# Kernel optimization log

Hardware: AMD Instinct MI355X
Metric: run time of the kernel (lower is better)

The kernel has to match this reference:

```python
import jax, jax.numpy as jnp
from jax import lax
import numpy as np

HEADS = 4
BUCKET = 64
DEPTH = 4


def _conv(x, w, b):
    y = lax.conv_general_dilated(x, w, (1, 1), [(1, 1), (1, 1)],
                                 dimension_numbers=('NCHW', 'OIHW', 'NCHW'))
    return y + b[None, :, None, None]


def _convT(x, w, b):
    # torch ConvTranspose2d(k=4, s=2, p=1): flip kernel, swap io, lhs_dilation=2, pad k-1-p=2
    wk = jnp.flip(w, (2, 3)).transpose(1, 0, 2, 3)
    y = lax.conv_general_dilated(x, wk, (1, 1), [(2, 2), (2, 2)], lhs_dilation=(2, 2),
                                 dimension_numbers=('NCHW', 'OIHW', 'NCHW'))
    return y + b[None, :, None, None]


def _maxpool(x):
    return lax.reduce_window(x, -jnp.inf, lax.max, (1, 1, 2, 2), (1, 1, 2, 2), 'VALID')


def _ln(x, g, b):
    m = x.mean(-1, keepdims=True)
    v = ((x - m) ** 2).mean(-1, keepdims=True)
    return (x - m) / jnp.sqrt(v + 1e-5) * g + b


def _lsh_attention(x, Wqk, bqk, Wv, bv, Wo, bo, rot):
    # shared-QK LSH bucketed attention (single hash round), look-one-back chunks
    B, N, D = x.shape
    h, dh = HEADS, D // HEADS
    qk = (x @ Wqk + bqk).reshape(B, N, h, dh).transpose(0, 2, 1, 3)  # B h N dh
    v = (x @ Wv + bv).reshape(B, N, h, dh).transpose(0, 2, 1, 3)
    k = qk / (jnp.linalg.norm(qk, axis=-1, keepdims=True) + 1e-6)    # keys = normalized queries
    rotated = jnp.einsum('bhnd,hdr->bhnr', qk, rot)
    buckets = jnp.argmax(jnp.concatenate([rotated, -rotated], -1), -1)  # B h N
    ticker = jnp.arange(N)
    perm = jnp.argsort(buckets * N + ticker, axis=-1)  # stable sort by bucket
    inv_perm = jnp.argsort(perm, axis=-1)
    g = lambda t: jnp.take_along_axis(t, perm[..., None], axis=2)
    nc = N // BUCKET
    bq = g(qk).reshape(B, h, nc, BUCKET, dh)
    bk = g(k).reshape(B, h, nc, BUCKET, dh)
    bv_ = g(v).reshape(B, h, nc, BUCKET, dh)
    bk2 = jnp.concatenate([bk, jnp.roll(bk, 1, axis=2)], axis=3)   # look one chunk back
    bv2 = jnp.concatenate([bv_, jnp.roll(bv_, 1, axis=2)], axis=3)
    dots = jnp.einsum('bhcid,bhcjd->bhcij', bq, bk2) * (dh ** -0.5)
    spos = jnp.take_along_axis(jnp.broadcast_to(ticker, buckets.shape), perm, -1).reshape(B, h, nc, BUCKET)
    kpos = jnp.concatenate([spos, jnp.roll(spos, 1, axis=2)], axis=3)
    dots = jnp.where(spos[..., :, None] == kpos[..., None, :], -1e5, dots)  # mask self (q == k)
    attn = jax.nn.softmax(dots, -1)
    o = jnp.einsum('bhcij,bhcjd->bhcid', attn, bv2).reshape(B, h, N, dh)
    o = jnp.take_along_axis(o, inv_perm[..., None], axis=2)  # unsort
    return o.transpose(0, 2, 1, 3).reshape(B, N, D) @ Wo + bo


def _reformer(seq, ln1_g, ln1_b, Wqk, bqk, Wv, bv, Wo, bo, rot, ln2_g, ln2_b, Wff1, bff1, Wff2, bff2):
    for i in range(DEPTH):
        seq = seq + _lsh_attention(_ln(seq, ln1_g[i], ln1_b[i]), Wqk[i], bqk[i], Wv[i], bv[i], Wo[i], bo[i], rot[i])
        hdn = jax.nn.gelu(_ln(seq, ln2_g[i], ln2_b[i]) @ Wff1[i] + bff1[i])
        seq = seq + hdn @ Wff2[i] + bff2[i]
    return seq


def _forward(burst, conv1_w, conv1_b, conv2_w, conv2_b, conv3_w, conv3_b,
             ln1_g, ln1_b, Wqk, bqk, Wv, bv, Wo, bo, rot, ln2_g, ln2_b,
             Wff1, bff1, Wff2, bff2, up1_w, up1_b, dec1_w, dec1_b,
             up2_w, up2_b, dec2_w, dec2_b, out_w, out_b):
    B, T, C, H, W = burst.shape
    x = burst.reshape(B * T, C, H, W)
    e1 = jax.nn.relu(_conv(x, conv1_w, conv1_b))
    p1 = _maxpool(e1)
    e2 = jax.nn.relu(_conv(p1, conv2_w, conv2_b))
    p2 = _maxpool(e2)
    bm = jax.nn.relu(_conv(p2, conv3_w, conv3_b))
    D = bm.shape[1]
    Hq, Wq = H // 4, W // 4
    seq = bm.transpose(0, 2, 3, 1).reshape(B * T, Hq * Wq, D)
    seq = _reformer(seq, ln1_g, ln1_b, Wqk, bqk, Wv, bv, Wo, bo, rot, ln2_g, ln2_b, Wff1, bff1, Wff2, bff2)
    bm = seq.reshape(B * T, Hq, Wq, D).transpose(0, 3, 1, 2)
    d1 = _convT(bm, up1_w, up1_b)
    d1 = jax.nn.relu(_conv(jnp.concatenate([d1, e2], 1), dec1_w, dec1_b))
    d2 = _convT(d1, up2_w, up2_b)
    d2 = jax.nn.relu(_conv(jnp.concatenate([d2, e1], 1), dec2_w, dec2_b))
    sharp = jax.nn.sigmoid(_conv(d2, out_w, out_b))
    return sharp.reshape(B, T, C, H, W)[:, 0]


def setup_inputs() -> dict:
    key = jax.random.key(0)
    ks = jax.random.split(key, 20)
    s = 0.05
    n = lambda k, shape: jax.random.normal(k, shape, jnp.float32) * s
    inp = {}
    inp['burst'] = jax.random.uniform(ks[0], (1, 7, 3, 256, 256), jnp.float32)
    inp['conv1_w'] = n(ks[1], (64, 3, 3, 3)); inp['conv1_b'] = jnp.zeros((64,), jnp.float32)
    inp['conv2_w'] = n(ks[2], (128, 64, 3, 3)); inp['conv2_b'] = jnp.zeros((128,), jnp.float32)
    inp['conv3_w'] = n(ks[3], (256, 128, 3, 3)); inp['conv3_b'] = jnp.zeros((256,), jnp.float32)
    inp['ln1_g'] = jnp.ones((4, 256), jnp.float32); inp['ln1_b'] = jnp.zeros((4, 256), jnp.float32)
    inp['Wqk'] = n(ks[4], (4, 256, 256)); inp['bqk'] = jnp.zeros((4, 256), jnp.float32)
    inp['Wv'] = n(ks[5], (4, 256, 256)); inp['bv'] = jnp.zeros((4, 256), jnp.float32)
    inp['Wo'] = n(ks[6], (4, 256, 256)); inp['bo'] = jnp.zeros((4, 256), jnp.float32)
    inp['rot'] = jax.random.normal(ks[7], (4, 4, 64, 32), jnp.float32)  # depth, heads, d_head, n_buckets//2
    inp['ln2_g'] = jnp.ones((4, 256), jnp.float32); inp['ln2_b'] = jnp.zeros((4, 256), jnp.float32)
    inp['Wff1'] = n(ks[8], (4, 256, 1024)); inp['bff1'] = jnp.zeros((4, 1024), jnp.float32)
    inp['Wff2'] = n(ks[9], (4, 1024, 256)); inp['bff2'] = jnp.zeros((4, 256), jnp.float32)
    inp['up1_w'] = n(ks[10], (256, 128, 4, 4)); inp['up1_b'] = jnp.zeros((128,), jnp.float32)
    inp['dec1_w'] = n(ks[11], (128, 256, 3, 3)); inp['dec1_b'] = jnp.zeros((128,), jnp.float32)
    inp['up2_w'] = n(ks[12], (128, 64, 4, 4)); inp['up2_b'] = jnp.zeros((64,), jnp.float32)
    inp['dec2_w'] = n(ks[13], (64, 128, 3, 3)); inp['dec2_b'] = jnp.zeros((64,), jnp.float32)
    inp['out_w'] = n(ks[14], (3, 64, 3, 3)); inp['out_b'] = jnp.zeros((3,), jnp.float32)
    return inp


def reference(burst, conv1_w, conv1_b, conv2_w, conv2_b, conv3_w, conv3_b,
              ln1_g, ln1_b, Wqk, bqk, Wv, bv, Wo, bo, rot, ln2_g, ln2_b,
              Wff1, bff1, Wff2, bff2, up1_w, up1_b, dec1_w, dec1_b,
              up2_w, up2_b, dec2_w, dec2_b, out_w, out_b):
    return _forward(burst, conv1_w, conv1_b, conv2_w, conv2_b, conv3_w, conv3_b,
                    ln1_g, ln1_b, Wqk, bqk, Wv, bv, Wo, bo, rot, ln2_g, ln2_b,
                    Wff1, bff1, Wff2, bff2, up1_w, up1_b, dec1_w, dec1_b,
                    up2_w, up2_b, dec2_w, dec2_b, out_w, out_b)
```

## Files before the change

### kernel.cpp

```cpp
#include <hip/hip_runtime.h>
#include <hip/hip_bf16.h>
#include <math.h>

using short8  = __attribute__((ext_vector_type(8))) short;
using half8   = __attribute__((ext_vector_type(8))) _Float16;
using floatx4 = __attribute__((ext_vector_type(4))) float;

static __device__ __forceinline__ float gelu_f(float x) {
    float x3 = x * x * x;
    return 0.5f * x * (1.f + tanhf(0.7978845608028654f * (x + 0.044715f * x3)));
}
static __device__ __forceinline__ short f2h(float f) {
    _Float16 h = (_Float16)f;
    return __builtin_bit_cast(short, h);
}
static __device__ __forceinline__ short f2bf(float f) {
    unsigned u = __float_as_uint(f);
    u += 0x7fffu + ((u >> 16) & 1u);
    return (short)(u >> 16);
}
static __device__ __forceinline__ float bf2f(short s) {
    return __uint_as_float(((unsigned)(unsigned short)s) << 16);
}
struct bf3s { short a, b, c; };
static __device__ __forceinline__ bf3s split3(float v) {
    short c0 = f2bf(v); float r = v - bf2f(c0);
    short c1 = f2bf(r); r -= bf2f(c1);
    short c2 = f2bf(r);
    bf3s s; s.a = c0; s.b = c1; s.c = c2; return s;
}

template <int OCB>
__global__ __launch_bounds__(256) void conv1_nhwc_kernel(
    const float* __restrict__ in1, const float* __restrict__ w,
    const float* __restrict__ bias, float* __restrict__ out, int H, int W, int OC)
{
    int tx = threadIdx.x, ty = threadIdx.y;
    int x = blockIdx.x * 16 + tx, y = blockIdx.y * 16 + ty;
    int oc0 = blockIdx.z * OCB;
    const int C = 3;
    float acc[OCB];
#pragma unroll
    for (int o = 0; o < OCB; ++o) acc[o] = 0.f;
    for (int ic = 0; ic < C; ++ic) {
        const float* src = in1 + (size_t)ic * H * W;
        float v[9];
#pragma unroll
        for (int ky = 0; ky < 3; ++ky) {
            int iy = y + ky - 1;
            bool okY = (iy >= 0) && (iy < H);
#pragma unroll
            for (int kx = 0; kx < 3; ++kx) {
                int ix = x + kx - 1;
                bool ok = okY && (ix >= 0) && (ix < W);
                v[ky * 3 + kx] = ok ? src[(size_t)iy * W + ix] : 0.f;
            }
        }
        const float* wp = w + ((size_t)oc0 * C + ic) * 9;
#pragma unroll
        for (int o = 0; o < OCB; ++o) {
            const float* wo = wp + (size_t)o * C * 9;
            acc[o] += v[0]*wo[0] + v[1]*wo[1] + v[2]*wo[2]
                    + v[3]*wo[3] + v[4]*wo[4] + v[5]*wo[5]
                    + v[6]*wo[6] + v[7]*wo[7] + v[8]*wo[8];
        }
    }
    float* op = out + ((size_t)y * W + x) * OC + oc0;
#pragma unroll
    for (int o = 0; o < OCB; ++o)
        op[o] = fmaxf(acc[o] + bias[oc0 + o], 0.f);
}

__global__ __launch_bounds__(256) void maxpool1_bf3_kernel(
    const float* __restrict__ in, short* __restrict__ o0, short* __restrict__ o1,
    short* __restrict__ o2, int OW, int IW, int C)
{
    int idx = blockIdx.x * 256 + threadIdx.x;
    int g = idx % (C >> 2); int p = idx / (C >> 2);
    int x = p % OW; int y = p / OW;
    size_t base = ((size_t)(2 * y) * IW + 2 * x) * C + g * 4;
    float4 a = *(const float4*)(in + base);
    float4 b = *(const float4*)(in + base + C);
    float4 c = *(const float4*)(in + base + (size_t)IW * C);
    float4 d = *(const float4*)(in + base + (size_t)IW * C + C);
    float v[4];
    v[0] = fmaxf(fmaxf(a.x, b.x), fmaxf(c.x, d.x));
    v[1] = fmaxf(fmaxf(a.y, b.y), fmaxf(c.y, d.y));
    v[2] = fmaxf(fmaxf(a.z, b.z), fmaxf(c.z, d.z));
    v[3] = fmaxf(fmaxf(a.w, b.w), fmaxf(c.w, d.w));
    size_t o = (size_t)p * C + g * 4;
#pragma unroll
    for (int j = 0; j < 4; ++j) {
        bf3s s = split3(v[j]);
        o0[o + j] = s.a; o1[o + j] = s.b; o2[o + j] = s.c;
    }
}

__global__ __launch_bounds__(256) void maxpool2_bf3_kernel(
    const short* __restrict__ i0, const short* __restrict__ i1,
    const short* __restrict__ i2, short* __restrict__ o0, short* __restrict__ o1,
    short* __restrict__ o2, int OW, int IW, int C)
{
    int idx = blockIdx.x * 256 + threadIdx.x;
    int g = idx % (C >> 2); int p = idx / (C >> 2);
    int x = p % OW; int y = p / OW;
    float v[4] = {-1e30f, -1e30f, -1e30f, -1e30f};
#pragma unroll
    for (int dy = 0; dy < 2; ++dy)
#pragma unroll
        for (int dx = 0; dx < 2; ++dx) {
            size_t base = ((size_t)(2 * y + dy) * IW + 2 * x + dx) * C + g * 4;
#pragma unroll
            for (int j = 0; j < 4; ++j) {
                float u = bf2f(i0[base + j]) + bf2f(i1[base + j]) + bf2f(i2[base + j]);
                v[j] = fmaxf(v[j], u);
            }
        }
    size_t o = (size_t)p * C + g * 4;
#pragma unroll
    for (int j = 0; j < 4; ++j) {
        bf3s s = split3(v[j]);
        o0[o + j] = s.a; o1[o + j] = s.b; o2[o + j] = s.c;
    }
}

__global__ void pack_conv3_kernel(const float* __restrict__ w,
                                  short* __restrict__ B0, short* __restrict__ B1,
                                  short* __restrict__ B2, int C, int OC, int total)
{
    int t = blockIdx.x * 256 + threadIdx.x;
    if (t >= total) return;
    int lane = t & 63, fi = t >> 6;
    int NT = OC >> 4;
    int nt = fi % NT, kt = fi / NT;
    int cpt = C >> 5;
    int tap = kt / cpt, ct = kt % cpt;
    int c = ct * 32 + (lane >> 4) * 8;
    int oc = nt * 16 + (lane & 15);
    short8 v0, v1, v2;
#pragma unroll
    for (int j = 0; j < 8; ++j) {
        bf3s s = split3(w[((size_t)oc * C + c + j) * 9 + tap]);
        v0[j] = s.a; v1[j] = s.b; v2[j] = s.c;
    }
    ((short8*)B0)[t] = v0; ((short8*)B1)[t] = v1; ((short8*)B2)[t] = v2;
}

__global__ __launch_bounds__(256) void conv_bf3_kernel(
    const short* __restrict__ ia0, const short* __restrict__ ia1,
    const short* __restrict__ ia2,
    const short* __restrict__ B0, const short* __restrict__ B1,
    const short* __restrict__ B2, const float* __restrict__ bias,
    float* __restrict__ outf, short* __restrict__ o0, short* __restrict__ o1,
    short* __restrict__ o2, short* __restrict__ oh,
    int H, int W, int C, int OC)
{
    int tid = threadIdx.x, wave = tid >> 6, lane = tid & 63;
    int quad = lane >> 4, l16 = lane & 15;
    int x0 = blockIdx.x * 64, y = blockIdx.y, nt0 = blockIdx.z * 4;
    int cpt = C >> 5, NT = OC >> 4;
    const short8* b0p = (const short8*)B0;
    const short8* b1p = (const short8*)B1;
    const short8* b2p = (const short8*)B2;
    floatx4 aM[4] = {{0,0,0,0},{0,0,0,0},{0,0,0,0},{0,0,0,0}};
    floatx4 aC[4] = {{0,0,0,0},{0,0,0,0},{0,0,0,0},{0,0,0,0}};
    int xm = x0 + wave * 16 + l16;
    for (int ky = 0; ky < 3; ++ky) {
        int yy = y + ky - 1;
        bool rok = (yy >= 0) && (yy < H);
        for (int kx = 0; kx < 3; ++kx) {
            int xx = xm + kx - 1;
            bool ok = rok && (xx >= 0) && (xx < W);
            size_t pos = (size_t)yy * W + xx;
            int ktb = (ky * 3 + kx) * cpt;
            for (int ct = 0; ct < cpt; ++ct) {
                int cc = ct * 32 + quad * 8;
                short8 A0 = {0,0,0,0,0,0,0,0}, A1 = A0, A2 = A0;
                if (ok) {
                    A0 = *(const short8*)(ia0 + pos * C + cc);
                    A1 = *(const short8*)(ia1 + pos * C + cc);
                    A2 = *(const short8*)(ia2 + pos * C + cc);
                }
                size_t bi = ((size_t)(ktb + ct) * NT + nt0) * 64 + lane;
#pragma unroll
                for (int s = 0; s < 4; ++s) {
                    short8 w0 = b0p[bi + s * 64];
                    short8 w1 = b1p[bi + s * 64];
                    short8 w2 = b2p[bi + s * 64];
                    aM[s] = __builtin_amdgcn_mfma_f32_16x16x32_bf16(A0, w0, aM[s], 0, 0, 0);
                    aC[s] = __builtin_amdgcn_mfma_f32_16x16x32_bf16(A0, w1, aC[s], 0, 0, 0);
                    aC[s] = __builtin_amdgcn_mfma_f32_16x16x32_bf16(A1, w0, aC[s], 0, 0, 0);
                    aC[s] = __builtin_amdgcn_mfma_f32_16x16x32_bf16(A0, w2, aC[s], 0, 0, 0);
                    aC[s] = __builtin_amdgcn_mfma_f32_16x16x32_bf16(A1, w1, aC[s], 0, 0, 0);
                    aC[s] = __builtin_amdgcn_mfma_f32_16x16x32_bf16(A2, w0, aC[s], 0, 0, 0);
                }
            }
        }
    }
#pragma unroll
    for (int s = 0; s < 4; ++s) {
        int n = (nt0 + s) * 16 + l16;
        float bs = bias[n];
#pragma unroll
        for (int r = 0; r < 4; ++r) {
            int m = wave * 16 + quad * 4 + r;
            int x = x0 + m;
            float v = fmaxf(aM[s][r] + aC[s][r] + bs, 0.f);
            size_t o = ((size_t)y * W + x) * OC + n;
            if (outf) outf[o] = v;
            else {
                bf3s sp = split3(v);
                o0[o] = sp.a; o1[o] = sp.b; o2[o] = sp.c;
                oh[o] = f2h(v);
            }
        }
    }
}

__global__ __launch_bounds__(256) void ln_bf3_kernel(
    const float* __restrict__ x, const float* __restrict__ g,
    const float* __restrict__ b, short* __restrict__ y0,
    short* __restrict__ y1, short* __restrict__ y2)
{
    int wave = threadIdx.x >> 6, lane = threadIdx.x & 63;
    int n = blockIdx.x * 4 + wave;
    const float* xr = x + (size_t)n * 256;
    float4 v = *(const float4*)(xr + lane * 4);
    float s = v.x + v.y + v.z + v.w;
#pragma unroll
    for (int m = 1; m < 64; m <<= 1) s += __shfl_xor(s, m);
    float mean = s * (1.f / 256.f);
    float cx = v.x - mean, cy = v.y - mean, cz = v.z - mean, cw = v.w - mean;
    float q = cx * cx + cy * cy + cz * cz + cw * cw;
#pragma unroll
    for (int m = 1; m < 64; m <<= 1) q += __shfl_xor(q, m);
    float rstd = rsqrtf(q * (1.f / 256.f) + 1e-5f);
    float4 gv = *(const float4*)(g + lane * 4);
    float4 bv = *(const float4*)(b + lane * 4);
    float o[4];
    o[0] = cx * rstd * gv.x + bv.x;
    o[1] = cy * rstd * gv.y + bv.y;
    o[2] = cz * rstd * gv.z + bv.z;
    o[3] = cw * rstd * gv.w + bv.w;
    size_t ob = (size_t)n * 256 + lane * 4;
#pragma unroll
    for (int j = 0; j < 4; ++j) {
        bf3s sp = split3(o[j]);
        y0[ob + j] = sp.a; y1[ob + j] = sp.b; y2[ob + j] = sp.c;
    }
}

__global__ __launch_bounds__(256) void bucketn_kernel(
    const float* __restrict__ qk, const float* __restrict__ rot,
    int* __restrict__ buckets, float* __restrict__ knrm)
{
    int t = blockIdx.x * 256 + threadIdx.x;
    int h = t >> 12, n = t & 4095;
    const float* q = qk + (size_t)n * 256 + h * 64;
    const float* R = rot + (size_t)h * 2048;
    float acc[32];
#pragma unroll
    for (int r = 0; r < 32; ++r) acc[r] = 0.f;
    float s2 = 0.f;
    for (int d = 0; d < 64; ++d) {
        float qd = q[d];
        s2 += qd * qd;
        const float* Rd = R + d * 32;
#pragma unroll
        for (int r = 0; r < 32; ++r) acc[r] += qd * Rd[r];
    }
    knrm[t] = 1.f / (sqrtf(s2) + 1e-6f);
    float bvv = acc[0]; int best = 0;
#pragma unroll
    for (int j = 1; j < 64; ++j) {
        float val = (j < 32) ? acc[j] : -acc[j - 32];
        if (val > bvv) { bvv = val; best = j; }
    }
    buckets[t] = best;
}

__global__ __launch_bounds__(256) void lsh_sort_kernel(
    const int* __restrict__ buckets, int* __restrict__ perm)
{
    int h = blockIdx.x;
    const int* bk = buckets + h * 4096;
    __shared__ unsigned long long mask[64][64];
    __shared__ int counts[64];
    __shared__ int offsets[64];
    __shared__ int wpre[64][64];
    int tid = threadIdx.x, wave = tid >> 6, lane = tid & 63;
    for (int w = wave * 16; w < wave * 16 + 16; ++w) {
        int bl = bk[w * 64 + lane];
        for (int b = 0; b < 64; ++b) {
            unsigned long long m = __ballot(bl == b);
            if (lane == b) mask[b][w] = m;
        }
    }
    __syncthreads();
    if (tid < 64) {
        int c = 0;
        for (int w = 0; w < 64; ++w) c += __popcll(mask[tid][w]);
        counts[tid] = c;
    }
    __syncthreads();
    if (tid == 0) {
        int a = 0;
        for (int b = 0; b < 64; ++b) { offsets[b] = a; a += counts[b]; }
    }
    __syncthreads();
    for (int b = wave * 16; b < wave * 16 + 16; ++b) {
        int c = __popcll(mask[b][lane]);
        int incl = c;
#pragma unroll
        for (int off = 1; off < 64; off <<= 1) {
            int nb = __shfl_up(incl, off);
            if (lane >= off) incl += nb;
        }
        wpre[b][lane] = incl - c + offsets[b];
    }
    __syncthreads();
    for (int i = tid; i < 4096; i += 256) {
        int b = bk[i]; int w = i >> 6; int l = i & 63;
        unsigned long long below = mask[b][w] & ((1ull << l) - 1ull);
        int pos = wpre[b][w] + __popcll(below);
        perm[h * 4096 + pos] = i;
    }
}

__global__ __launch_bounds__(256) void attn_kernel(
    const float* __restrict__ qk, const float* __restrict__ vv,
    const float* __restrict__ knrm, const int* __restrict__ perm,
    short* __restrict__ o0, short* __restrict__ o1, short* __restrict__ o2)
{
    __shared__ float ks[128 * 64];
    __shared__ float dotsT[128 * 64];
    int c = blockIdx.x, h = blockIdx.y;
    int tid = threadIdx.x;
    const int* pm = perm + h * 4096;
    int cm = (c + 63) & 63;
    {
        int jr = tid >> 1, hf = tid & 1;
        int sk = (jr < 64) ? (c * 64 + jr) : (cm * 64 + (jr - 64));
        int nk = pm[sk];
        float sc = knrm[h * 4096 + nk];
        const float* src = qk + (size_t)nk * 256 + h * 64 + hf * 32;
        float* dst = ks + jr * 64 + hf * 32;
#pragma unroll
        for (int d = 0; d < 32; d += 4) {
            float4 v = *(const float4*)(src + d);
            v.x *= sc; v.y *= sc; v.z *= sc; v.w *= sc;
            *(float4*)(dst + d) = v;
        }
    }
    __syncthreads();
    int r = tid & 63, jg = tid >> 6;
    int nq = pm[c * 64 + r];
    {
        float qreg[64];
        const float* src = qk + (size_t)nq * 256 + h * 64;
#pragma unroll
        for (int d = 0; d < 64; d += 4) {
            float4 v = *(const float4*)(src + d);
            qreg[d] = v.x; qreg[d + 1] = v.y; qreg[d + 2] = v.z; qreg[d + 3] = v.w;
        }
        for (int j = jg * 32; j < jg * 32 + 32; ++j) {
            const float* kr = ks + j * 64;
            float dot = 0.f;
#pragma unroll
            for (int d = 0; d < 64; ++d) dot += qreg[d] * kr[d];
            int sk = (j < 64) ? (c * 64 + j) : (cm * 64 + (j - 64));
            int nk = pm[sk];
            dot = (nk == nq) ? -1e5f : dot * 0.125f;
            dotsT[j * 64 + r] = dot;
        }
    }
    __syncthreads();
    {
        int jr = tid >> 1, hf = tid & 1;
        int sk = (jr < 64) ? (c * 64 + jr) : (cm * 64 + (jr - 64));
        int nk = pm[sk];
        const float* src = vv + (size_t)nk * 256 + h * 64 + hf * 32;
        float* dst = ks + jr * 64 + hf * 32;
#pragma unroll
        for (int d = 0; d < 32; d += 4)
            *(float4*)(dst + d) = *(const float4*)(src + d);
    }
    if (tid < 64) {
        int rr = tid;
        float mx = -1e30f;
        for (int j = 0; j < 128; ++j) mx = fmaxf(mx, dotsT[j * 64 + rr]);
        float s = 0.f;
        for (int j = 0; j < 128; ++j) {
            float e = expf(dotsT[j * 64 + rr] - mx);
            dotsT[j * 64 + rr] = e; s += e;
        }
        float inv = 1.f / s;
        for (int j = 0; j < 128; ++j) dotsT[j * 64 + rr] *= inv;
    }
    __syncthreads();
    int dg = jg;
    float acc[16];
#pragma unroll
    for (int d = 0; d < 16; ++d) acc[d] = 0.f;
    for (int j = 0; j < 128; ++j) {
        float a = dotsT[j * 64 + r];
        const float* vr = ks + j * 64 + dg * 16;
#pragma unroll
        for (int d = 0; d < 16; ++d) acc[d] += a * vr[d];
    }
    size_t ob = (size_t)nq * 256 + h * 64 + dg * 16;
#pragma unroll
    for (int d = 0; d < 16; ++d) {
        bf3s sp = split3(acc[d]);
        o0[ob + d] = sp.a; o1[ob + d] = sp.b; o2[ob + d] = sp.c;
    }
}

static __device__ __forceinline__ void pack_one(
    const float* __restrict__ W, short* __restrict__ B0, short* __restrict__ B1,
    short* __restrict__ B2, int N, int t)
{
    int lane = t & 63, fi = t >> 6;
    int NT = N >> 4;
    int nt = fi % NT, kt = fi / NT;
    int n = nt * 16 + (lane & 15);
    int k0 = kt * 32 + (lane >> 4) * 8;
    short8 v0, v1, v2;
#pragma unroll
    for (int j = 0; j < 8; ++j) {
        bf3s s = split3(W[(size_t)(k0 + j) * N + n]);
        v0[j] = s.a; v1[j] = s.b; v2[j] = s.c;
    }
    ((short8*)B0)[t] = v0; ((short8*)B1)[t] = v1; ((short8*)B2)[t] = v2;
}

__global__ void pack_layer_kernel(
    const float* __restrict__ Wqk, const float* __restrict__ Wv,
    const float* __restrict__ Wo, const float* __restrict__ Wff1,
    const float* __restrict__ Wff2,
    short* q0, short* q1, short* q2, short* v0, short* v1, short* v2,
    short* o0, short* o1, short* o2, short* f10, short* f11, short* f12,
    short* f20, short* f21, short* f22)
{
    int t = blockIdx.x * 256 + threadIdx.x;
    if (t < 8192)       pack_one(Wqk, q0, q1, q2, 256, t);
    else if (t < 16384) pack_one(Wv, v0, v1, v2, 256, t - 8192);
    else if (t < 24576) pack_one(Wo, o0, o1, o2, 256, t - 16384);
    else if (t < 57344) pack_one(Wff1, f10, f11, f12, 1024, t - 24576);
    else if (t < 90112) pack_one(Wff2, f20, f21, f22, 256, t - 57344);
}

static __device__ __forceinline__ void gemm_bf3_core(
    const short* __restrict__ A0, const short* __restrict__ A1,
    const short* __restrict__ A2,
    const short* __restrict__ B0, const short* __restrict__ B1,
    const short* __restrict__ B2, const float* __restrict__ bias,
    float* __restrict__ Cf, short* __restrict__ D0, short* __restrict__ D1,
    short* __restrict__ D2, int N, int K, int act, int resid, int bx, int by)
{
    int tid = threadIdx.x, wave = tid >> 6, lane = tid & 63;
    int quad = lane >> 4, l16 = lane & 15;
    int m0 = by * 64 + wave * 16;
    int NT = N >> 4, nt0 = bx * 2;
    size_t arow = (size_t)(m0 + l16) * K + quad * 8;
    const short8* b0p = (const short8*)B0;
    const short8* b1p = (const short8*)B1;
    const short8* b2p = (const short8*)B2;
    floatx4 aM0 = {0,0,0,0}, aM1 = {0,0,0,0};
    floatx4 aC10 = {0,0,0,0}, aC11 = {0,0,0,0};
    floatx4 aC20 = {0,0,0,0}, aC21 = {0,0,0,0};
    int KT = K >> 5;
    size_t bi0 = (size_t)nt0 * 64 + lane;
    short8 a0 = *(const short8*)(A0 + arow);
    short8 a1 = *(const short8*)(A1 + arow);
    short8 a2 = *(const short8*)(A2 + arow);
    short8 w00 = b0p[bi0], w01 = b1p[bi0], w02 = b2p[bi0];
    short8 w10 = b0p[bi0 + 64], w11 = b1p[bi0 + 64], w12 = b2p[bi0 + 64];
    for (int kt = 0; kt < KT; ++kt) {
        short8 na0 = {}, na1 = {}, na2 = {};
        short8 nw00 = {}, nw01 = {}, nw02 = {}, nw10 = {}, nw11 = {}, nw12 = {};
        if (kt + 1 < KT) {
            size_t ar = arow + (size_t)(kt + 1) * 32;
            na0 = *(const short8*)(A0 + ar);
            na1 = *(const short8*)(A1 + ar);
            na2 = *(const short8*)(A2 + ar);
            size_t nbi = ((size_t)(kt + 1) * NT + nt0) * 64 + lane;
            nw00 = b0p[nbi]; nw01 = b1p[nbi]; nw02 = b2p[nbi];
            nw10 = b0p[nbi + 64]; nw11 = b1p[nbi + 64]; nw12 = b2p[nbi + 64];
        }
        aM0  = __builtin_amdgcn_mfma_f32_16x16x32_bf16(a0, w00, aM0, 0, 0, 0);
        aM1  = __builtin_amdgcn_mfma_f32_16x16x32_bf16(a0, w10, aM1, 0, 0, 0);
        aC10 = __builtin_amdgcn_mfma_f32_16x16x32_bf16(a0, w01, aC10, 0, 0, 0);
        aC11 = __builtin_amdgcn_mfma_f32_16x16x32_bf16(a0, w11, aC11, 0, 0, 0);
        aC20 = __builtin_amdgcn_mfma_f32_16x16x32_bf16(a1, w00, aC20, 0, 0, 0);
        aC21 = __builtin_amdgcn_mfma_f32_16x16x32_bf16(a1, w10, aC21, 0, 0, 0);
        aC10 = __builtin_amdgcn_mfma_f32_16x16x32_bf16(a0, w02, aC10, 0, 0, 0);
        aC11 = __builtin_amdgcn_mfma_f32_16x16x32_bf16(a0, w12, aC11, 0, 0, 0);
        aC20 = __builtin_amdgcn_mfma_f32_16x16x32_bf16(a1, w01, aC20, 0, 0, 0);
        aC21 = __builtin_amdgcn_mfma_f32_16x16x32_bf16(a1, w11, aC21, 0, 0, 0);
        aC10 = __builtin_amdgcn_mfma_f32_16x16x32_bf16(a2, w00, aC10, 0, 0, 0);
        aC11 = __builtin_amdgcn_mfma_f32_16x16x32_bf16(a2, w10, aC11, 0, 0, 0);
        a0 = na0; a1 = na1; a2 = na2;
        w00 = nw00; w01 = nw01; w02 = nw02;
        w10 = nw10; w11 = nw11; w12 = nw12;
    }
    floatx4 aM[2] = {aM0, aM1};
    floatx4 c1[2] = {aC10, aC11};
    floatx4 c2[2] = {aC20, aC21};
#pragma unroll
    for (int s = 0; s < 2; ++s) {
        int n = (nt0 + s) * 16 + l16;
        float bs = bias[n];
#pragma unroll
        for (int r = 0; r < 4; ++r) {
            int m = m0 + quad * 4 + r;
            float v = aM[s][r] + (c1[s][r] + c2[s][r]) + bs;
            if (act == 1) v = gelu_f(v);
            size_t o = (size_t)m * N + n;
            if (D0) {
                bf3s sp = split3(v);
                D0[o] = sp.a; D1[o] = sp.b; D2[o] = sp.c;
            } else {
                if (resid) v += Cf[o];
                Cf[o] = v;
            }
        }
    }
}

__global__ __launch_bounds__(256) void gemm_bf3_kernel(
    const short* A0, const short* A1, const short* A2,
    const short* B0, const short* B1, const short* B2,
    const float* bias, float* Cf, short* D0, short* D1, short* D2,
    int N, int K, int act, int resid)
{
    gemm_bf3_core(A0, A1, A2, B0, B1, B2, bias, Cf, D0, D1, D2,
                  N, K, act, resid, blockIdx.x, blockIdx.y);
}

__global__ __launch_bounds__(256) void gemm_qkv_bf3_kernel(
    const short* A0, const short* A1, const short* A2,
    const short* Q0, const short* Q1, const short* Q2,
    const float* qb, float* Cq,
    const short* V0, const short* V1, const short* V2,
    const float* vb, float* Cv, int K)
{
    int side = blockIdx.x >> 3;
    gemm_bf3_core(A0, A1, A2, side ? V0 : Q0, side ? V1 : Q1, side ? V2 : Q2,
                  side ? vb : qb, side ? Cv : Cq, nullptr, nullptr, nullptr,
                  256, K, 0, 0, blockIdx.x & 7, blockIdx.y);
}

__global__ void pack_conv_kernel(const float* __restrict__ w, short* __restrict__ Bp,
                                 int C, int OC, int NT, int total)
{
    int t = blockIdx.x * 256 + threadIdx.x;
    if (t >= total) return;
    int lane = t & 63, fi = t >> 6;
    int nt = fi % NT, kt = fi / NT;
    int cpt = C >> 5;
    int tap = kt / cpt, ct = kt % cpt;
    int c = ct * 32 + (lane >> 4) * 8;
    int oc = nt * 16 + (lane & 15);
    short8 v;
#pragma unroll
    for (int j = 0; j < 8; ++j) {
        float f = (oc < OC) ? w[((size_t)oc * C + c + j) * 9 + tap] : 0.f;
        v[j] = f2h(f);
    }
    ((short8*)Bp)[t] = v;
}

__global__ void pack_convt_kernel(const float* __restrict__ w, short* __restrict__ Bp,
                                  int IC, int OC, int total)
{
    int t = blockIdx.x * 256 + threadIdx.x;
    if (t >= total) return;
    int lane = t & 63, fi = t >> 6;
    int NT = OC >> 4, cpt = IC >> 5, KT4 = 4 * cpt;
    int nt = fi % NT, r = fi / NT;
    int kt = r % KT4, pz = r / KT4;
    int py = pz >> 1, px = pz & 1;
    int t4 = kt / cpt, ct = kt % cpt;
    int ty = t4 >> 1, tx = t4 & 1;
    int ky = py ? (2 * ty) : (1 + 2 * ty);
    int kx = px ? (2 * tx) : (1 + 2 * tx);
    int ic = ct * 32 + (lane >> 4) * 8;
    int oc = nt * 16 + (lane & 15);
    short8 v;
#pragma unroll
    for (int j = 0; j < 8; ++j)
        v[j] = f2h(w[(((size_t)(ic + j) * OC + oc) * 4 + ky) * 4 + kx]);
    ((short8*)Bp)[t] = v;
}

__global__ __launch_bounds__(256) void conv_mfma_kernel(
    const short* __restrict__ in1, int C1, const short* __restrict__ in2, int C2,
    const short* __restrict__ Bp, const float* __restrict__ bias,
    short* __restrict__ outb, int H, int W, int OC)
{
    int tid = threadIdx.x, wave = tid >> 6, lane = tid & 63;
    int quad = lane >> 4, l16 = lane & 15;
    int x0 = blockIdx.x * 64, y = blockIdx.y, nt0 = blockIdx.z * 4;
    int C = C1 + C2, cpt = C >> 5, NT = OC >> 4;
    const half8* bp = (const half8*)Bp;
    floatx4 acc[4] = {{0,0,0,0},{0,0,0,0},{0,0,0,0},{0,0,0,0}};
    int xm = x0 + wave * 16 + l16;
    for (int ky = 0; ky < 3; ++ky) {
        int yy = y + ky - 1;
        bool rok = (yy >= 0) && (yy < H);
        for (int kx = 0; kx < 3; ++kx) {
            int xx = xm + kx - 1;
            bool ok = rok && (xx >= 0) && (xx < W);
            size_t pos = (size_t)yy * W + xx;
            int ktb = (ky * 3 + kx) * cpt;
            for (int ct = 0; ct < cpt; ++ct) {
                int cc = ct * 32 + quad * 8;
                half8 a = {};
                if (ok) {
                    const short* src = (cc < C1) ? (in1 + pos * C1 + cc)
                                                 : (in2 + pos * C2 + (cc - C1));
                    a = *(const half8*)src;
                }
                size_t bi = ((size_t)(ktb + ct) * NT + nt0) * 64 + lane;
#pragma unroll
                for (int s = 0; s < 4; ++s)
                    acc[s] = __builtin_amdgcn_mfma_f32_16x16x32_f16(a, bp[bi + s * 64], acc[s], 0, 0, 0);
            }
        }
    }
#pragma unroll
    for (int s = 0; s < 4; ++s) {
        int n = (nt0 + s) * 16 + l16;
        float bs = bias[n];
#pragma unroll
        for (int r = 0; r < 4; ++r) {
            int m = wave * 16 + quad * 4 + r;
            int x = x0 + m;
            float v = fmaxf(acc[s][r] + bs, 0.f);
            outb[((size_t)y * W + x) * OC + n] = f2h(v);
        }
    }
}

__global__ __launch_bounds__(256) void convt_mfma_kernel(
    const short* __restrict__ in, int IC, const short* __restrict__ Bp,
    const float* __restrict__ bias, short* __restrict__ outb, int IH, int IW, int OC)
{
    int tid = threadIdx.x, wave = tid >> 6, lane = tid & 63;
    int quad = lane >> 4, l16 = lane & 15;
    int pz = blockIdx.z & 3, nt0 = (blockIdx.z >> 2) * 4;
    int py = pz >> 1, px = pz & 1;
    int a0 = blockIdx.y, b0 = blockIdx.x * 64;
    int cpt = IC >> 5, NT = OC >> 4, KT4 = 4 * cpt;
    const half8* bp = (const half8*)Bp;
    floatx4 acc[4] = {{0,0,0,0},{0,0,0,0},{0,0,0,0},{0,0,0,0}};
    int bm = b0 + wave * 16 + l16;
    for (int ty = 0; ty < 2; ++ty) {
        int iy = a0 + (py ? (1 - ty) : (-ty));
        bool rok = (iy >= 0) && (iy < IH);
        for (int tx = 0; tx < 2; ++tx) {
            int ix = bm + (px ? (1 - tx) : (-tx));
            bool ok = rok && (ix >= 0) && (ix < IW);
            size_t pos = (size_t)iy * IW + ix;
            int ktb = (ty * 2 + tx) * cpt;
            for (int ct = 0; ct < cpt; ++ct) {
                int cc = ct * 32 + quad * 8;
                half8 a = {};
                if (ok) a = *(const half8*)(in + pos * IC + cc);
                size_t bi = ((size_t)(pz * KT4 + ktb + ct) * NT + nt0) * 64 + lane;
#pragma unroll
                for (int s = 0; s < 4; ++s)
                    acc[s] = __builtin_amdgcn_mfma_f32_16x16x32_f16(a, bp[bi + s * 64], acc[s], 0, 0, 0);
            }
        }
    }
    int OW = IW * 2;
    int oy = 2 * a0 + py;
#pragma unroll
    for (int s = 0; s < 4; ++s) {
        int n = (nt0 + s) * 16 + l16;
        float bs = bias[n];
#pragma unroll
        for (int r = 0; r < 4; ++r) {
            int m = wave * 16 + quad * 4 + r;
            int ox = 2 * (b0 + m) + px;
            outb[((size_t)oy * OW + ox) * OC + n] = f2h(acc[s][r] + bs);
        }
    }
}

__global__ __launch_bounds__(256) void convout_mfma_kernel(
    const short* __restrict__ in, const short* __restrict__ Bp,
    const float* __restrict__ bias, float* __restrict__ out, int H, int W)
{
    int tid = threadIdx.x, wave = tid >> 6, lane = tid & 63;
    int quad = lane >> 4, l16 = lane & 15;
    int x0 = blockIdx.x * 64, y = blockIdx.y;
    const int C = 64, cpt = 2;
    const half8* bp = (const half8*)Bp;
    floatx4 acc = {0,0,0,0};
    int xm = x0 + wave * 16 + l16;
    for (int ky = 0; ky < 3; ++ky) {
        int yy = y + ky - 1;
        bool rok = (yy >= 0) && (yy < H);
        for (int kx = 0; kx < 3; ++kx) {
            int xx = xm + kx - 1;
            bool ok = rok && (xx >= 0) && (xx < W);
            size_t pos = (size_t)yy * W + xx;
            int ktb = (ky * 3 + kx) * cpt;
#pragma unroll
            for (int ct = 0; ct < cpt; ++ct) {
                int cc = ct * 32 + quad * 8;
                half8 a = {};
                if (ok) a = *(const half8*)(in + pos * C + cc);
                acc = __builtin_amdgcn_mfma_f32_16x16x32_f16(
                          a, bp[(size_t)(ktb + ct) * 64 + lane], acc, 0, 0, 0);
            }
        }
    }
    int oc = l16;
    if (oc < 3) {
        float bs = bias[oc];
#pragma unroll
        for (int r = 0; r < 4; ++r) {
            int m = wave * 16 + quad * 4 + r;
            int x = x0 + m;
            float v = acc[r] + bs;
            out[(size_t)oc * H * W + (size_t)y * W + x] = 1.f / (1.f + expf(-v));
        }
    }
}

__global__ __launch_bounds__(256) void f2h_kernel(
    const float* __restrict__ in, short* __restrict__ out, int n)
{
    int i = blockIdx.x * 256 + threadIdx.x;
    if (i < n) out[i] = f2h(in[i]);
}

extern "C" void kernel_launch(void* const* d_in, const int* in_sizes, int n_in,
                              void* d_out, int out_size, void* d_ws, size_t ws_size,
                              hipStream_t stream)
{
    const float* burst   = (const float*)d_in[0];
    const float* conv1_w = (const float*)d_in[1];  const float* conv1_b = (const float*)d_in[2];
    const float* conv2_w = (const float*)d_in[3];  const float* conv2_b = (const float*)d_in[4];
    const float* conv3_w = (const float*)d_in[5];  const float* conv3_b = (const float*)d_in[6];
    const float* ln1_g   = (const float*)d_in[7];  const float* ln1_b   = (const float*)d_in[8];
    const float* Wqk     = (const float*)d_in[9];  const float* bqk     = (const float*)d_in[10];
    const float* Wv      = (const float*)d_in[11]; const float* bvv     = (const float*)d_in[12];
    const float* Wo      = (const float*)d_in[13]; const float* bo      = (const float*)d_in[14];
    const float* rot     = (const float*)d_in[15];
    const float* ln2_g   = (const float*)d_in[16]; const float* ln2_b   = (const float*)d_in[17];
    const float* Wff1    = (const float*)d_in[18]; const float* bff1    = (const float*)d_in[19];
    const float* Wff2    = (const float*)d_in[20]; const float* bff2    = (const float*)d_in[21];
    const float* up1_w   = (const float*)d_in[22]; const float* up1_b   = (const float*)d_in[23];
    const float* dec1_w  = (const float*)d_in[24]; const float* dec1_b  = (const float*)d_in[25];
    const float* up2_w   = (const float*)d_in[26]; const float* up2_b   = (const float*)d_in[27];
    const float* dec2_w  = (const float*)d_in[28]; const float* dec2_b  = (const float*)d_in[29];
    const float* out_w   = (const float*)d_in[30]; const float* out_b   = (const float*)d_in[31];

    float* ws = (float*)d_ws;
    short* e1h = (short*)(ws + 0);
    short* e2h = (short*)(ws + 2097152);
    float* seq = ws + 3145728;
    float* qkb = ws + 4194304;
    float* vvb = ws + 5242880;
    float* knb = ws + 6291456;
    int* buckets = (int*)(ws + 6307840);
    int* perm    = (int*)(ws + 6324224);
    short* xn0 = (short*)(ws + 6340608);
    short* xn1 = (short*)(ws + 6864896);
    short* xn2 = (short*)(ws + 7389184);
    short* hdn0 = (short*)(ws + 7913472);
    short* hdn1 = (short*)(ws + 10010624);
    short* hdn2 = (short*)(ws + 12107776);
    short* pqk0 = (short*)(ws + 14204928); short* pqk1 = (short*)(ws + 14237696); short* pqk2 = (short*)(ws + 14270464);
    short* pv0  = (short*)(ws + 14303232); short* pv1  = (short*)(ws + 14336000); short* pv2  = (short*)(ws + 14368768);
    short* po0  = (short*)(ws + 14401536); short* po1  = (short*)(ws + 14434304); short* po2  = (short*)(ws + 14467072);
    short* pf10 = (short*)(ws + 14499840); short* pf11 = (short*)(ws + 14630912); short* pf12 = (short*)(ws + 14761984);
    short* pf20 = (short*)(ws + 14893056); short* pf21 = (short*)(ws + 15024128); short* pf22 = (short*)(ws + 15155200);
    short* pdec1 = (short*)(ws + 15286272);
    short* pdec2 = (short*)(ws + 15433728);
    short* pout  = (short*)(ws + 15470592);
    short* pup1  = (short*)(ws + 15475200);
    short* pup2  = (short*)(ws + 15737344);
    float* e1f = ws + 7913472;
    short* p1_0 = (short*)(ws + 12107776); short* p1_1 = (short*)(ws + 12632064); short* p1_2 = (short*)(ws + 13156352);
    short* p2_0 = (short*)(ws + 13680640); short* p2_1 = (short*)(ws + 13942784); short* p2_2 = (short*)(ws + 14204928);
    short* pc2_0 = (short*)(ws + 14467072); short* pc2_1 = (short*)(ws + 14503936); short* pc2_2 = (short*)(ws + 14540800);
    short* pc3_0 = (short*)(ws + 14577664); short* pc3_1 = (short*)(ws + 14725120); short* pc3_2 = (short*)(ws + 14872576);
    short* e2_0 = (short*)(ws + 4194304); short* e2_1 = (short*)(ws + 5242880); short* e2_2 = (short*)(ws + 6291456);
    short* seqh = (short*)(ws + 7913472);
    short* d1   = (short*)(ws + 8437760);
    short* d1c  = (short*)(ws + 9486336);
    short* d2   = (short*)(ws + 10534912);
    short* d2c  = (short*)(ws + 12632064);

    dim3 b16(16, 16);

    pack_conv3_kernel<<<36, 256, 0, stream>>>(conv2_w, pc2_0, pc2_1, pc2_2, 64, 128, 9216);
    pack_conv3_kernel<<<144, 256, 0, stream>>>(conv3_w, pc3_0, pc3_1, pc3_2, 128, 256, 36864);
    pack_conv_kernel<<<144, 256, 0, stream>>>(dec1_w, pdec1, 256, 128, 8, 36864);
    pack_conv_kernel<<<36, 256, 0, stream>>>(dec2_w, pdec2, 128, 64, 4, 9216);
    pack_conv_kernel<<<5, 256, 0, stream>>>(out_w, pout, 64, 3, 1, 1152);
    pack_convt_kernel<<<256, 256, 0, stream>>>(up1_w, pup1, 256, 128, 65536);
    pack_convt_kernel<<<64, 256, 0, stream>>>(up2_w, pup2, 128, 64, 16384);

    conv1_nhwc_kernel<8><<<dim3(16, 16, 8), b16, 0, stream>>>(
        burst, conv1_w, conv1_b, e1f, 256, 256, 64);
    f2h_kernel<<<16384, 256, 0, stream>>>(e1f, e1h, 4194304);
    maxpool1_bf3_kernel<<<1024, 256, 0, stream>>>(e1f, p1_0, p1_1, p1_2, 128, 256, 64);
    conv_bf3_kernel<<<dim3(2, 128, 2), 256, 0, stream>>>(
        p1_0, p1_1, p1_2, pc2_0, pc2_1, pc2_2, conv2_b,
        nullptr, e2_0, e2_1, e2_2, e2h, 128, 128, 64, 128);
    maxpool2_bf3_kernel<<<512, 256, 0, stream>>>(
        e2_0, e2_1, e2_2, p2_0, p2_1, p2_2, 64, 128, 128);
    conv_bf3_kernel<<<dim3(1, 64, 4), 256, 0, stream>>>(
        p2_0, p2_1, p2_2, pc3_0, pc3_1, pc3_2, conv3_b,
        seq, nullptr, nullptr, nullptr, nullptr, 64, 64, 128, 256);

    for (int i = 0; i < 4; ++i) {
        pack_layer_kernel<<<352, 256, 0, stream>>>(
            Wqk + i * 65536, Wv + i * 65536, Wo + i * 65536,
            Wff1 + i * 262144, Wff2 + i * 262144,
            pqk0, pqk1, pqk2, pv0, pv1, pv2, po0, po1, po2,
            pf10, pf11, pf12, pf20, pf21, pf22);
        ln_bf3_kernel<<<1024, 256, 0, stream>>>(seq, ln1_g + i * 256, ln1_b + i * 256,
                                                xn0, xn1, xn2);
        gemm_qkv_bf3_kernel<<<dim3(16, 64), 256, 0, stream>>>(
            xn0, xn1, xn2, pqk0, pqk1, pqk2, bqk + i * 256, qkb,
            pv0, pv1, pv2, bvv + i * 256, vvb, 256);
        bucketn_kernel<<<64, 256, 0, stream>>>(qkb, rot + i * 8192, buckets, knb);
        lsh_sort_kernel<<<4, 256, 0, stream>>>(buckets, perm);
        attn_kernel<<<dim3(64, 4), 256, 0, stream>>>(qkb, vvb, knb, perm, xn0, xn1, xn2);
        gemm_bf3_kernel<<<dim3(8, 64), 256, 0, stream>>>(
            xn0, xn1, xn2, po0, po1, po2, bo + i * 256, seq,
            nullptr, nullptr, nullptr, 256, 256, 0, 1);
        ln_bf3_kernel<<<1024, 256, 0, stream>>>(seq, ln2_g + i * 256, ln2_b + i * 256,
                                                xn0, xn1, xn2);
        gemm_bf3_kernel<<<dim3(32, 64), 256, 0, stream>>>(
            xn0, xn1, xn2, pf10, pf11, pf12, bff1 + i * 1024, nullptr,
            hdn0, hdn1, hdn2, 1024, 256, 1, 0);
        gemm_bf3_kernel<<<dim3(8, 64), 256, 0, stream>>>(
            hdn0, hdn1, hdn2, pf20, pf21, pf22, bff2 + i * 256, seq,
            nullptr, nullptr, nullptr, 256, 1024, 0, 1);
    }

    f2h_kernel<<<4096, 256, 0, stream>>>(seq, seqh, 1048576);
    convt_mfma_kernel<<<dim3(1, 64, 8), 256, 0, stream>>>(
        seqh, 256, pup1, up1_b, d1, 64, 64, 128);
    conv_mfma_kernel<<<dim3(2, 128, 2), 256, 0, stream>>>(
        d1, 128, e2h, 128, pdec1, dec1_b, d1c, 128, 128, 128);
    convt_mfma_kernel<<<dim3(2, 128, 4), 256, 0, stream>>>(
        d1c, 128, pup2, up2_b, d2, 128, 128, 64);
    conv_mfma_kernel<<<dim3(4, 256, 1), 256, 0, stream>>>(
        d2, 64, e1h, 64, pdec2, dec2_b, d2c, 256, 256, 64);
    convout_mfma_kernel<<<dim3(4, 256), 256, 0, stream>>>(
        d2c, pout, out_b, (float*)d_out, 256, 256);
}
```

Baseline: 1.379 ms.

## Split attention rows across blocks with parallel softmax; fuse fp16 casts into producers

The attention kernel now splits each chunk's 64 query rows over two blocks, giving 512 blocks. The softmax max and sum are computed by all 256 threads through per-group partial reductions instead of 64 threads looping serially, and normalisation is folded into the output scaling. The two standalone f2h conversion kernels are removed: conv1 and the last FF2 GEMM now write the fp16 copy directly. This trades extra K/V loads per chunk (each block reloads the full 128 keys) for more parallelism and fewer launches and memory passes.

```diff
diff --git a/kernel.cpp b/kernel.cpp
--- a/kernel.cpp
+++ b/kernel.cpp
@@ -33,7 +33,8 @@
 template <int OCB>
 __global__ __launch_bounds__(256) void conv1_nhwc_kernel(
     const float* __restrict__ in1, const float* __restrict__ w,
-    const float* __restrict__ bias, float* __restrict__ out, int H, int W, int OC)
+    const float* __restrict__ bias, float* __restrict__ out,
+    short* __restrict__ outh, int H, int W, int OC)
 {
     int tx = threadIdx.x, ty = threadIdx.y;
     int x = blockIdx.x * 16 + tx, y = blockIdx.y * 16 + ty;
@@ -65,10 +66,13 @@
                     + v[6]*wo[6] + v[7]*wo[7] + v[8]*wo[8];
         }
     }
-    float* op = out + ((size_t)y * W + x) * OC + oc0;
-#pragma unroll
-    for (int o = 0; o < OCB; ++o)
-        op[o] = fmaxf(acc[o] + bias[oc0 + o], 0.f);
+    size_t ob = ((size_t)y * W + x) * OC + oc0;
+#pragma unroll
+    for (int o = 0; o < OCB; ++o) {
+        float r = fmaxf(acc[o] + bias[oc0 + o], 0.f);
+        out[ob + o] = r;
+        outh[ob + o] = f2h(r);
+    }
 }
 
 __global__ __launch_bounds__(256) void maxpool1_bf3_kernel(
@@ -333,8 +337,10 @@
     short* __restrict__ o0, short* __restrict__ o1, short* __restrict__ o2)
 {
     __shared__ float ks[128 * 64];
-    __shared__ float dotsT[128 * 64];
-    int c = blockIdx.x, h = blockIdx.y;
+    __shared__ float dotsT[128 * 32];
+    __shared__ float pmax[8][32];
+    __shared__ float psum[8][32];
+    int c = blockIdx.x, h = blockIdx.y, rh = blockIdx.z;
     int tid = threadIdx.x;
     const int* pm = perm + h * 4096;
     int cm = (c + 63) & 63;
@@ -353,8 +359,10 @@
         }
     }
     __syncthreads();
-    int r = tid & 63, jg = tid >> 6;
+    int rr = tid & 31, jq = tid >> 5;
+    int r = rh * 32 + rr;
     int nq = pm[c * 64 + r];
+    float mx = -1e30f;
     {
         float qreg[64];
         const float* src = qk + (size_t)nq * 256 + h * 64;
@@ -363,18 +371,36 @@
             float4 v = *(const float4*)(src + d);
             qreg[d] = v.x; qreg[d + 1] = v.y; qreg[d + 2] = v.z; qreg[d + 3] = v.w;
         }
-        for (int j = jg * 32; j < jg * 32 + 32; ++j) {
+        for (int jj = 0; jj < 16; ++jj) {
+            int j = jq * 16 + jj;
             const float* kr = ks + j * 64;
             float dot = 0.f;
 #pragma unroll
-            for (int d = 0; d < 64; ++d) dot += qreg[d] * kr[d];
+            for (int d = 0; d < 64; d += 4) {
+                float4 kv = *(const float4*)(kr + d);
+                dot += qreg[d] * kv.x + qreg[d + 1] * kv.y
+                     + qreg[d + 2] * kv.z + qreg[d + 3] * kv.w;
+            }
             int sk = (j < 64) ? (c * 64 + j) : (cm * 64 + (j - 64));
             int nk = pm[sk];
             dot = (nk == nq) ? -1e5f : dot * 0.125f;
-            dotsT[j * 64 + r] = dot;
-        }
-    }
+            dotsT[j * 32 + rr] = dot;
+            mx = fmaxf(mx, dot);
+        }
+    }
+    pmax[jq][rr] = mx;
     __syncthreads();
+    float gmax = pmax[0][rr];
+#pragma unroll
+    for (int g = 1; g < 8; ++g) gmax = fmaxf(gmax, pmax[g][rr]);
+    float ss = 0.f;
+    for (int jj = 0; jj < 16; ++jj) {
+        int j = jq * 16 + jj;
+        float e = expf(dotsT[j * 32 + rr] - gmax);
+        dotsT[j * 32 + rr] = e;
+        ss += e;
+    }
+    psum[jq][rr] = ss;
     {
         int jr = tid >> 1, hf = tid & 1;
         int sk = (jr < 64) ? (c * 64 + jr) : (cm * 64 + (jr - 64));
@@ -385,33 +411,24 @@
         for (int d = 0; d < 32; d += 4)
             *(float4*)(dst + d) = *(const float4*)(src + d);
     }
-    if (tid < 64) {
-        int rr = tid;
-        float mx = -1e30f;
-        for (int j = 0; j < 128; ++j) mx = fmaxf(mx, dotsT[j * 64 + rr]);
-        float s = 0.f;
-        for (int j = 0; j < 128; ++j) {
-            float e = expf(dotsT[j * 64 + rr] - mx);
-            dotsT[j * 64 + rr] = e; s += e;
-        }
-        float inv = 1.f / s;
-        for (int j = 0; j < 128; ++j) dotsT[j * 64 + rr] *= inv;
-    }
     __syncthreads();
-    int dg = jg;
-    float acc[16];
-#pragma unroll
-    for (int d = 0; d < 16; ++d) acc[d] = 0.f;
+    float tot = psum[0][rr];
+#pragma unroll
+    for (int g = 1; g < 8; ++g) tot += psum[g][rr];
+    float inv = 1.f / tot;
+    float acc[8] = {0.f, 0.f, 0.f, 0.f, 0.f, 0.f, 0.f, 0.f};
     for (int j = 0; j < 128; ++j) {
-        float a = dotsT[j * 64 + r];
-        const float* vr = ks + j * 64 + dg * 16;
-#pragma unroll
-        for (int d = 0; d < 16; ++d) acc[d] += a * vr[d];
-    }
-    size_t ob = (size_t)nq * 256 + h * 64 + dg * 16;
-#pragma unroll
-    for (int d = 0; d < 16; ++d) {
-        bf3s sp = split3(acc[d]);
+        float a = dotsT[j * 32 + rr];
+        const float* vr = ks + j * 64 + jq * 8;
+        float4 v0 = *(const float4*)(vr);
+        float4 v1 = *(const float4*)(vr + 4);
+        acc[0] += a * v0.x; acc[1] += a * v0.y; acc[2] += a * v0.z; acc[3] += a * v0.w;
+        acc[4] += a * v1.x; acc[5] += a * v1.y; acc[6] += a * v1.z; acc[7] += a * v1.w;
+    }
+    size_t ob = (size_t)nq * 256 + h * 64 + jq * 8;
+#pragma unroll
+    for (int d = 0; d < 8; ++d) {
+        bf3s sp = split3(acc[d] * inv);
         o0[ob + d] = sp.a; o1[ob + d] = sp.b; o2[ob + d] = sp.c;
     }
 }
@@ -456,7 +473,8 @@
     const short* __restrict__ B0, const short* __restrict__ B1,
     const short* __restrict__ B2, const float* __restrict__ bias,
     float* __restrict__ Cf, short* __restrict__ D0, short* __restrict__ D1,
-    short* __restrict__ D2, int N, int K, int act, int resid, int bx, int by)
+    short* __restrict__ D2, short* __restrict__ Dh,
+    int N, int K, int act, int resid, int bx, int by)
 {
     int tid = threadIdx.x, wave = tid >> 6, lane = tid & 63;
     int quad = lane >> 4, l16 = lane & 15;
@@ -523,6 +541,7 @@
             } else {
                 if (resid) v += Cf[o];
                 Cf[o] = v;
+                if (Dh) Dh[o] = f2h(v);
             }
         }
     }
@@ -531,10 +550,10 @@
 __global__ __launch_bounds__(256) void gemm_bf3_kernel(
     const short* A0, const short* A1, const short* A2,
     const short* B0, const short* B1, const short* B2,
-    const float* bias, float* Cf, short* D0, short* D1, short* D2,
+    const float* bias, float* Cf, short* D0, short* D1, short* D2, short* Dh,
     int N, int K, int act, int resid)
 {
-    gemm_bf3_core(A0, A1, A2, B0, B1, B2, bias, Cf, D0, D1, D2,
+    gemm_bf3_core(A0, A1, A2, B0, B1, B2, bias, Cf, D0, D1, D2, Dh,
                   N, K, act, resid, blockIdx.x, blockIdx.y);
 }
 
@@ -548,7 +567,7 @@
     int side = blockIdx.x >> 3;
     gemm_bf3_core(A0, A1, A2, side ? V0 : Q0, side ? V1 : Q1, side ? V2 : Q2,
                   side ? vb : qb, side ? Cv : Cq, nullptr, nullptr, nullptr,
-                  256, K, 0, 0, blockIdx.x & 7, blockIdx.y);
+                  nullptr, 256, K, 0, 0, blockIdx.x & 7, blockIdx.y);
 }
 
 __global__ void pack_conv_kernel(const float* __restrict__ w, short* __restrict__ Bp,
@@ -730,13 +749,6 @@
             out[(size_t)oc * H * W + (size_t)y * W + x] = 1.f / (1.f + expf(-v));
         }
     }
-}
-
-__global__ __launch_bounds__(256) void f2h_kernel(
-    const float* __restrict__ in, short* __restrict__ out, int n)
-{
-    int i = blockIdx.x * 256 + threadIdx.x;
-    if (i < n) out[i] = f2h(in[i]);
 }
 
 extern "C" void kernel_launch(void* const* d_in, const int* in_sizes, int n_in,
@@ -809,8 +821,7 @@
     pack_convt_kernel<<<64, 256, 0, stream>>>(up2_w, pup2, 128, 64, 16384);
 
     conv1_nhwc_kernel<8><<<dim3(16, 16, 8), b16, 0, stream>>>(
-        burst, conv1_w, conv1_b, e1f, 256, 256, 64);
-    f2h_kernel<<<16384, 256, 0, stream>>>(e1f, e1h, 4194304);
+        burst, conv1_w, conv1_b, e1f, e1h, 256, 256, 64);
     maxpool1_bf3_kernel<<<1024, 256, 0, stream>>>(e1f, p1_0, p1_1, p1_2, 128, 256, 64);
     conv_bf3_kernel<<<dim3(2, 128, 2), 256, 0, stream>>>(
         p1_0, p1_1, p1_2, pc2_0, pc2_1, pc2_2, conv2_b,
@@ -834,21 +845,20 @@
             pv0, pv1, pv2, bvv + i * 256, vvb, 256);
         bucketn_kernel<<<64, 256, 0, stream>>>(qkb, rot + i * 8192, buckets, knb);
         lsh_sort_kernel<<<4, 256, 0, stream>>>(buckets, perm);
-        attn_kernel<<<dim3(64, 4), 256, 0, stream>>>(qkb, vvb, knb, perm, xn0, xn1, xn2);
+        attn_kernel<<<dim3(64, 4, 2), 256, 0, stream>>>(qkb, vvb, knb, perm, xn0, xn1, xn2);
         gemm_bf3_kernel<<<dim3(8, 64), 256, 0, stream>>>(
             xn0, xn1, xn2, po0, po1, po2, bo + i * 256, seq,
-            nullptr, nullptr, nullptr, 256, 256, 0, 1);
+            nullptr, nullptr, nullptr, nullptr, 256, 256, 0, 1);
         ln_bf3_kernel<<<1024, 256, 0, stream>>>(seq, ln2_g + i * 256, ln2_b + i * 256,
                                                 xn0, xn1, xn2);
         gemm_bf3_kernel<<<dim3(32, 64), 256, 0, stream>>>(
             xn0, xn1, xn2, pf10, pf11, pf12, bff1 + i * 1024, nullptr,
-            hdn0, hdn1, hdn2, 1024, 256, 1, 0);
+            hdn0, hdn1, hdn2, nullptr, 1024, 256, 1, 0);
         gemm_bf3_kernel<<<dim3(8, 64), 256, 0, stream>>>(
             hdn0, hdn1, hdn2, pf20, pf21, pf22, bff2 + i * 256, seq,
-            nullptr, nullptr, nullptr, 256, 1024, 0, 1);
-    }
-
-    f2h_kernel<<<4096, 256, 0, stream>>>(seq, seqh, 1048576);
+            nullptr, nullptr, nullptr, (i == 3) ? seqh : nullptr, 256, 1024, 0, 1);
+    }
+
     convt_mfma_kernel<<<dim3(1, 64, 8), 256, 0, stream>>>(
         seqh, 256, pup1, up1_b, d1, 64, 64, 128);
     conv_mfma_kernel<<<dim3(2, 128, 2), 256, 0, stream>>>(
```

After: 1.321 ms. -4.2%, faster.
